# Kernel optimization log

Hardware: AMD Instinct MI355X
Metric: run time of the kernel (lower is better)

Reference implementation:

```python
import jax, jax.numpy as jnp
import numpy as np
from jax import lax

C = 512
B, T, N = 8, 16, 32
KSZ = 7
NEG_SLOPE = 0.01
LN_EPS = 1e-5


def setup_inputs() -> dict:
    key = jax.random.key(0)
    ks = jax.random.split(key, 8)
    local_feat = jax.random.normal(ks[0], (B, T, N, C), dtype=jnp.float32)
    global_feat = jax.random.normal(ks[1], (B, C), dtype=jnp.float32)
    pos = jax.random.normal(ks[2], (B, T, N, 3), dtype=jnp.float32)
    # adj_weight: nn.Linear(C, C, bias=False), init eye_ (perturb slightly to keep interesting ties)
    W = jnp.eye(C, dtype=jnp.float32) + 0.01 * jax.random.normal(ks[3], (C, C), dtype=jnp.float32)
    # depthwise Conv1d(C, C, 7, groups=C): weight [C, 1, 7], kaiming init; bias zeros
    conv_w = jax.random.normal(ks[4], (C, 1, KSZ), dtype=jnp.float32) * np.sqrt(2.0 / KSZ)
    conv_b = jnp.zeros((C,), dtype=jnp.float32)
    ln_gamma = jnp.ones((C,), dtype=jnp.float32)
    ln_beta = jnp.zeros((C,), dtype=jnp.float32)
    return {"local_feat": local_feat, "global_feat": global_feat, "pos": pos,
            "W": W, "conv_w": conv_w, "conv_b": conv_b,
            "ln_gamma": ln_gamma, "ln_beta": ln_beta}


def reference(local_feat, global_feat, pos, W, conv_w, conv_b, ln_gamma, ln_beta):
    b, t, nd, c = local_feat.shape
    n = t * nd
    feat = local_feat.reshape(b, n, c)
    # F.normalize(p=2, dim=-1, eps=1e-12)
    norm = feat / jnp.maximum(jnp.linalg.norm(feat, axis=-1, keepdims=True), 1e-12)
    # torch.einsum('bnc,cc,bcm->bnm'): repeated 'cc' takes the diagonal of W
    A = jnp.einsum('bnc,cc,bcm->bnm', norm, W, jnp.swapaxes(norm, 1, 2))
    A = A.reshape(b, n, t, nd)
    top_A = jnp.argmax(A, axis=-1)  # [b, n, t]
    # direct indexed gather -- avoids the [b, n, t, nd, c] stacked blowup
    top_feat = local_feat[jnp.arange(b)[:, None, None],
                          jnp.arange(t)[None, None, :],
                          top_A]                                 # [b, n, t, c]
    x = jnp.swapaxes(top_feat.reshape(b * n, t, c), 1, 2)        # [b*n, c, t]
    # depthwise conv1d, kernel 7, valid padding
    y = lax.conv_general_dilated(x, conv_w, window_strides=(1,), padding='VALID',
                                 dimension_numbers=('NCH', 'OIH', 'NCH'),
                                 feature_group_count=c)
    y = y + conv_b[None, :, None]                                # [b*n, c, t-6]
    y = jnp.swapaxes(y, 1, 2)                                    # [b*n, t-6, c]
    mu = jnp.mean(y, axis=-1, keepdims=True)
    var = jnp.mean(jnp.square(y - mu), axis=-1, keepdims=True)
    ln = (y - mu) * lax.rsqrt(var + LN_EPS) * ln_gamma + ln_beta
    act = jnp.where(ln >= 0, ln, NEG_SLOPE * ln)
    out = jnp.mean(act, axis=1)                                  # mean over time -> [b*n, c]
    return out.reshape(b, t, nd, c)
```

## Files before the change

### kernel.cpp

```cpp
#include <hip/hip_runtime.h>
#include <hip/hip_bf16.h>

#define C_DIM 512
#define B_DIM 8
#define T_DIM 16
#define ND_DIM 32
#define NPTS 512
#define ROWS 4096
#define KSZ 7
#define TOUT 10
#define NEG_SLOPE 0.01f
#define LN_EPS 1e-5f

__global__ __launch_bounds__(256) void norm_kernel(const float* __restrict__ feat,
                                                   float* __restrict__ nrm) {
    int row = blockIdx.x;
    int tid = threadIdx.x;
    const float* f = feat + (size_t)row * C_DIM;
    float* o = nrm + (size_t)row * C_DIM;
    float v0 = f[tid];
    float v1 = f[tid + 256];
    float ss = v0 * v0 + v1 * v1;
    #pragma unroll
    for (int off = 32; off > 0; off >>= 1) ss += __shfl_down(ss, off, 64);
    __shared__ float wsum[4];
    int wid = tid >> 6, lane = tid & 63;
    if (lane == 0) wsum[wid] = ss;
    __syncthreads();
    float tot = wsum[0] + wsum[1] + wsum[2] + wsum[3];
    float inv = 1.0f / fmaxf(sqrtf(tot), 1e-12f);
    o[tid] = v0 * inv;
    o[tid + 256] = v1 * inv;
}

__global__ __launch_bounds__(256, 1) void gemm_part_kernel(const float* __restrict__ nrm,
                                                           const float* __restrict__ W,
                                                           float* __restrict__ part) {
    __shared__ __align__(16) float As[2][128][20];
    __shared__ __align__(16) float Bs[2][128][20];
    __shared__ float wd[256];
    const int tid = threadIdx.x;
    const int tx = tid & 15, ty = tid >> 4;
    const int b = blockIdx.z >> 1, kz = blockIdx.z & 1;
    const int row0 = blockIdx.y * 128, col0 = blockIdx.x * 128;
    const int kbase = kz * 256;
    const float* __restrict__ Nb = nrm + (size_t)b * NPTS * C_DIM;

    wd[tid] = W[(size_t)(kbase + tid) * (C_DIM + 1)];
    __syncthreads();

    const int sr = tid >> 1;
    const int kh = (tid & 1) * 8;

    {
        const float* ga = Nb + (size_t)(row0 + sr) * C_DIM + kbase + kh;
        const float* gb = Nb + (size_t)(col0 + sr) * C_DIM + kbase + kh;
        float4 a0 = *(const float4*)ga, a1 = *(const float4*)(ga + 4);
        float4 b0 = *(const float4*)gb, b1 = *(const float4*)(gb + 4);
        float4 w0 = *(const float4*)&wd[kh], w1 = *(const float4*)&wd[kh + 4];
        a0.x *= w0.x; a0.y *= w0.y; a0.z *= w0.z; a0.w *= w0.w;
        a1.x *= w1.x; a1.y *= w1.y; a1.z *= w1.z; a1.w *= w1.w;
        *(float4*)&As[0][sr][kh] = a0; *(float4*)&As[0][sr][kh + 4] = a1;
        *(float4*)&Bs[0][sr][kh] = b0; *(float4*)&Bs[0][sr][kh + 4] = b1;
    }

    float acc[8][8] = {};
    #pragma unroll 1
    for (int step = 0; step < 16; ++step) {
        __syncthreads();
        const int buf = step & 1;
        if (step + 1 < 16) {
            const int koff = (step + 1) * 16;
            const float* ga = Nb + (size_t)(row0 + sr) * C_DIM + kbase + koff + kh;
            const float* gb = Nb + (size_t)(col0 + sr) * C_DIM + kbase + koff + kh;
            float4 a0 = *(const float4*)ga, a1 = *(const float4*)(ga + 4);
            float4 b0 = *(const float4*)gb, b1 = *(const float4*)(gb + 4);
            float4 w0 = *(const float4*)&wd[koff + kh], w1 = *(const float4*)&wd[koff + kh + 4];
            a0.x *= w0.x; a0.y *= w0.y; a0.z *= w0.z; a0.w *= w0.w;
            a1.x *= w1.x; a1.y *= w1.y; a1.z *= w1.z; a1.w *= w1.w;
            *(float4*)&As[buf ^ 1][sr][kh] = a0; *(float4*)&As[buf ^ 1][sr][kh + 4] = a1;
            *(float4*)&Bs[buf ^ 1][sr][kh] = b0; *(float4*)&Bs[buf ^ 1][sr][kh + 4] = b1;
        }
        #pragma unroll
        for (int k4 = 0; k4 < 4; ++k4) {
            float4 av[8], bv[8];
            #pragma unroll
            for (int i = 0; i < 8; i++) av[i] = *(const float4*)&As[buf][ty + 16 * i][k4 * 4];
            #pragma unroll
            for (int j = 0; j < 8; j++) bv[j] = *(const float4*)&Bs[buf][tx + 16 * j][k4 * 4];
            #pragma unroll
            for (int i = 0; i < 8; i++)
                #pragma unroll
                for (int j = 0; j < 8; j++)
                    acc[i][j] += av[i].x * bv[j].x + av[i].y * bv[j].y
                               + av[i].z * bv[j].z + av[i].w * bv[j].w;
        }
    }

    float* Cb = part + ((size_t)(kz * B_DIM + b) * NPTS + row0) * NPTS + col0;
    #pragma unroll
    for (int i = 0; i < 8; i++)
        #pragma unroll
        for (int j = 0; j < 8; j++)
            Cb[(size_t)(ty + 16 * i) * NPTS + tx + 16 * j] = acc[i][j];
}

__global__ __launch_bounds__(256) void reduce_argmax_kernel(const float* __restrict__ part,
                                                            int* __restrict__ idxg) {
    const int bn = blockIdx.x * 4 + (threadIdx.x >> 6);
    const int lane = threadIdx.x & 63;
    const float* p0 = part + (size_t)bn * NPTS + lane * 8;
    const float* p1 = part + (size_t)(ROWS + bn) * NPTS + lane * 8;
    float4 x0 = *(const float4*)p0, x1 = *(const float4*)(p0 + 4);
    float4 y0 = *(const float4*)p1, y1 = *(const float4*)(p1 + 4);
    float v[8] = { x0.x + y0.x, x0.y + y0.y, x0.z + y0.z, x0.w + y0.w,
                   x1.x + y1.x, x1.y + y1.y, x1.z + y1.z, x1.w + y1.w };
    float best = v[0];
    int bc = lane * 8;
    #pragma unroll
    for (int c = 1; c < 8; c++) {
        if (v[c] > best) { best = v[c]; bc = lane * 8 + c; }
    }
    #pragma unroll
    for (int m = 1; m < 4; m <<= 1) {
        float ov = __shfl_xor(best, m, 64);
        int oc = __shfl_xor(bc, m, 64);
        if (ov > best || (ov == best && oc < bc)) { best = ov; bc = oc; }
    }
    if ((lane & 3) == 0) idxg[(size_t)bn * T_DIM + (lane >> 2)] = bc & 31;
}

__global__ __launch_bounds__(256) void gemm_argmax_kernel(const float* __restrict__ nrm,
                                                          const float* __restrict__ W,
                                                          int* __restrict__ idxg) {
    __shared__ __align__(16) float As[16][68];
    __shared__ __align__(16) float Bs[16][68];
    __shared__ float Cs[64][65];
    __shared__ float wd[C_DIM];
    const int tid = threadIdx.x;
    const int tx = tid & 15, ty = tid >> 4;
    const int b = blockIdx.z;
    const int row0 = blockIdx.y * 64, col0 = blockIdx.x * 64;
    const float* Nb = nrm + (size_t)b * NPTS * C_DIM;

    wd[tid]       = W[(size_t)tid * (C_DIM + 1)];
    wd[tid + 256] = W[(size_t)(tid + 256) * (C_DIM + 1)];
    __syncthreads();

    float acc[4][4] = {};
    for (int k0 = 0; k0 < C_DIM; k0 += 16) {
        #pragma unroll
        for (int e = 0; e < 4; e++) {
            int idx = tid + e * 256;
            int m = idx >> 4, kk = idx & 15;
            As[kk][m] = Nb[(size_t)(row0 + m) * C_DIM + k0 + kk] * wd[k0 + kk];
            Bs[kk][m] = Nb[(size_t)(col0 + m) * C_DIM + k0 + kk];
        }
        __syncthreads();
        #pragma unroll
        for (int kk = 0; kk < 16; kk++) {
            float4 a4 = *(const float4*)&As[kk][ty * 4];
            float4 b4 = *(const float4*)&Bs[kk][tx * 4];
            float av[4] = {a4.x, a4.y, a4.z, a4.w};
            float bv[4] = {b4.x, b4.y, b4.z, b4.w};
            #pragma unroll
            for (int i = 0; i < 4; i++)
                #pragma unroll
                for (int j = 0; j < 4; j++)
                    acc[i][j] += av[i] * bv[j];
        }
        __syncthreads();
    }
    #pragma unroll
    for (int i = 0; i < 4; i++)
        #pragma unroll
        for (int j = 0; j < 4; j++)
            Cs[ty * 4 + i][tx * 4 + j] = acc[i][j];
    __syncthreads();
    if (tid < 128) {
        int r = tid >> 1, g = tid & 1;
        const float* crow = &Cs[r][g * 32];
        float best = crow[0];
        int bi = 0;
        for (int j = 1; j < 32; j++) {
            float v = crow[j];
            if (v > best) { best = v; bi = j; }
        }
        int n_glob = b * NPTS + row0 + r;
        int tg = (col0 >> 5) + g;
        idxg[(size_t)n_glob * T_DIM + tg] = bi;
    }
}

__global__ __launch_bounds__(256, 2) void fuse_kernel(const int* __restrict__ idxg,
                                                      const float* __restrict__ lf,
                                                      const float* __restrict__ cw,
                                                      const float* __restrict__ cb,
                                                      const float* __restrict__ gamma,
                                                      const float* __restrict__ beta,
                                                      float* __restrict__ out) {
    const int wave = threadIdx.x >> 6;
    const int lane = threadIdx.x & 63;
    const int bn = blockIdx.x * 4 + wave;
    const int b = bn >> 9;
    const int c0 = lane * 8;

    float x[T_DIM][8];
    #pragma unroll
    for (int t = 0; t < T_DIM; t++) {
        int idx = idxg[(size_t)bn * T_DIM + t];
        const float* p = lf + (((size_t)(b * T_DIM + t)) * ND_DIM + idx) * C_DIM + c0;
        float4 lo = *(const float4*)p;
        float4 hi = *(const float4*)(p + 4);
        x[t][0] = lo.x; x[t][1] = lo.y; x[t][2] = lo.z; x[t][3] = lo.w;
        x[t][4] = hi.x; x[t][5] = hi.y; x[t][6] = hi.z; x[t][7] = hi.w;
    }

    float w[KSZ][8];
    #pragma unroll
    for (int c = 0; c < 8; c++)
        #pragma unroll
        for (int k = 0; k < KSZ; k++)
            w[k][c] = cw[(size_t)(c0 + c) * KSZ + k];
    float bias[8], g[8], be[8];
    {
        float4 b_lo = *(const float4*)&cb[c0],    b_hi = *(const float4*)&cb[c0 + 4];
        float4 g_lo = *(const float4*)&gamma[c0], g_hi = *(const float4*)&gamma[c0 + 4];
        float4 e_lo = *(const float4*)&beta[c0],  e_hi = *(const float4*)&beta[c0 + 4];
        bias[0]=b_lo.x; bias[1]=b_lo.y; bias[2]=b_lo.z; bias[3]=b_lo.w;
        bias[4]=b_hi.x; bias[5]=b_hi.y; bias[6]=b_hi.z; bias[7]=b_hi.w;
        g[0]=g_lo.x; g[1]=g_lo.y; g[2]=g_lo.z; g[3]=g_lo.w;
        g[4]=g_hi.x; g[5]=g_hi.y; g[6]=g_hi.z; g[7]=g_hi.w;
        be[0]=e_lo.x; be[1]=e_lo.y; be[2]=e_lo.z; be[3]=e_lo.w;
        be[4]=e_hi.x; be[5]=e_hi.y; be[6]=e_hi.z; be[7]=e_hi.w;
    }

    float accum[8] = {};
    #pragma unroll
    for (int tau = 0; tau < TOUT; tau++) {
        float y[8];
        #pragma unroll
        for (int c = 0; c < 8; c++) {
            float v = bias[c];
            #pragma unroll
            for (int k = 0; k < KSZ; k++) v += x[tau + k][c] * w[k][c];
            y[c] = v;
        }
        float s = 0.f, q = 0.f;
        #pragma unroll
        for (int c = 0; c < 8; c++) { s += y[c]; q += y[c] * y[c]; }
        #pragma unroll
        for (int m = 1; m < 64; m <<= 1) {
            s += __shfl_xor(s, m, 64);
            q += __shfl_xor(q, m, 64);
        }
        float mu = s * (1.0f / 512.0f);
        float var = q * (1.0f / 512.0f) - mu * mu;
        float rs = rsqrtf(var + LN_EPS);
        #pragma unroll
        for (int c = 0; c < 8; c++) {
            float ln = (y[c] - mu) * rs * g[c] + be[c];
            accum[c] += ln >= 0.f ? ln : NEG_SLOPE * ln;
        }
    }
    float* o = out + (size_t)bn * C_DIM + c0;
    float4 r_lo = make_float4(accum[0]*0.1f, accum[1]*0.1f, accum[2]*0.1f, accum[3]*0.1f);
    float4 r_hi = make_float4(accum[4]*0.1f, accum[5]*0.1f, accum[6]*0.1f, accum[7]*0.1f);
    *(float4*)o = r_lo;
    *(float4*)(o + 4) = r_hi;
}

__global__ void sentinel_kernel(float* out, int n, float val) {
    int i = blockIdx.x * 256 + threadIdx.x;
    if (i < n) out[i] = val;
}

extern "C" void kernel_launch(void* const* d_in, const int* in_sizes, int n_in,
                              void* d_out, int out_size, void* d_ws, size_t ws_size,
                              hipStream_t stream) {
    const float* local_feat = (const float*)d_in[0];
    const float* W       = (const float*)d_in[3];
    const float* conv_w  = (const float*)d_in[4];
    const float* conv_b  = (const float*)d_in[5];
    const float* ln_g    = (const float*)d_in[6];
    const float* ln_b    = (const float*)d_in[7];
    float* out = (float*)d_out;

    (void)hipGetLastError();

    const size_t nrm_bytes  = (size_t)ROWS * C_DIM * sizeof(float);
    const size_t part_bytes = (size_t)2 * ROWS * NPTS * sizeof(float);
    const size_t idx_bytes  = (size_t)ROWS * T_DIM * sizeof(int);

    if (d_ws == nullptr || ws_size < nrm_bytes + idx_bytes) {
        float val = 512.0f + (float)(ws_size >> 20);
        sentinel_kernel<<<(out_size + 255) / 256, 256, 0, stream>>>(out, out_size, val);
        return;
    }

    float* nrm = (float*)d_ws;

    norm_kernel<<<ROWS, 256, 0, stream>>>(local_feat, nrm);

    int* idxg;
    if (ws_size >= nrm_bytes + part_bytes + idx_bytes) {
        float* part = (float*)((char*)d_ws + nrm_bytes);
        idxg = (int*)((char*)d_ws + nrm_bytes + part_bytes);
        gemm_part_kernel<<<dim3(NPTS / 128, NPTS / 128, B_DIM * 2), 256, 0, stream>>>(nrm, W, part);
        reduce_argmax_kernel<<<ROWS / 4, 256, 0, stream>>>(part, idxg);
    } else {
        idxg = (int*)((char*)d_ws + nrm_bytes);
        gemm_argmax_kernel<<<dim3(NPTS / 64, NPTS / 64, B_DIM), 256, 0, stream>>>(nrm, W, idxg);
    }

    fuse_kernel<<<ROWS / 4, 256, 0, stream>>>(idxg, local_feat, conv_w, conv_b,
                                              ln_g, ln_b, out);

    if (hipGetLastError() != hipSuccess) {
        hipMemsetAsync(d_out, 0x42, (size_t)out_size * 2, stream);
    }
}
```

Baseline: 150.7 us.

## Fold row normalization into GEMM loads and split K four ways

Replaces the normalized-feature materialization with a small kernel that computes only per-row inverse norms, which the GEMM applies while loading raw features. The K dimension is split four ways instead of two, doubling GEMM block count, and launch bounds now allow two blocks per CU. The reduce kernel sums four partial slices. This avoids writing and rereading the 8 MB normalized tensor but doubles the size of the partial-product buffer the reduce must read.

```diff
diff --git a/kernel.cpp b/kernel.cpp
--- a/kernel.cpp
+++ b/kernel.cpp
@@ -11,6 +11,21 @@
 #define TOUT 10
 #define NEG_SLOPE 0.01f
 #define LN_EPS 1e-5f
+#define KZ 4
+
+__global__ __launch_bounds__(256) void rnorm_kernel(const float* __restrict__ feat,
+                                                    float* __restrict__ rn) {
+    const int row = blockIdx.x * 4 + (threadIdx.x >> 6);
+    const int lane = threadIdx.x & 63;
+    const float* f = feat + (size_t)row * C_DIM + lane * 8;
+    float4 a = *(const float4*)f;
+    float4 b = *(const float4*)(f + 4);
+    float ss = a.x*a.x + a.y*a.y + a.z*a.z + a.w*a.w
+             + b.x*b.x + b.y*b.y + b.z*b.z + b.w*b.w;
+    #pragma unroll
+    for (int m = 1; m < 64; m <<= 1) ss += __shfl_xor(ss, m, 64);
+    if (lane == 0) rn[row] = 1.0f / fmaxf(sqrtf(ss), 1e-12f);
+}
 
 __global__ __launch_bounds__(256) void norm_kernel(const float* __restrict__ feat,
                                                    float* __restrict__ nrm) {
@@ -33,30 +48,36 @@
     o[tid + 256] = v1 * inv;
 }
 
-__global__ __launch_bounds__(256, 1) void gemm_part_kernel(const float* __restrict__ nrm,
+__global__ __launch_bounds__(256, 2) void gemm_part_kernel(const float* __restrict__ feat,
+                                                           const float* __restrict__ rn,
                                                            const float* __restrict__ W,
                                                            float* __restrict__ part) {
     __shared__ __align__(16) float As[2][128][20];
     __shared__ __align__(16) float Bs[2][128][20];
-    __shared__ float wd[256];
+    __shared__ float wd[128];
     const int tid = threadIdx.x;
     const int tx = tid & 15, ty = tid >> 4;
-    const int b = blockIdx.z >> 1, kz = blockIdx.z & 1;
+    const int b = blockIdx.z >> 2, kz = blockIdx.z & 3;
     const int row0 = blockIdx.y * 128, col0 = blockIdx.x * 128;
-    const int kbase = kz * 256;
-    const float* __restrict__ Nb = nrm + (size_t)b * NPTS * C_DIM;
-
-    wd[tid] = W[(size_t)(kbase + tid) * (C_DIM + 1)];
-    __syncthreads();
+    const int kbase = kz * 128;
+
+    if (tid < 128) wd[tid] = W[(size_t)(kbase + tid) * (C_DIM + 1)];
 
     const int sr = tid >> 1;
     const int kh = (tid & 1) * 8;
+    const float* __restrict__ fA = feat + (size_t)(b * NPTS + row0 + sr) * C_DIM + kbase + kh;
+    const float* __restrict__ fB = feat + (size_t)(b * NPTS + col0 + sr) * C_DIM + kbase + kh;
+    const float rna = rn[b * NPTS + row0 + sr];
+    const float rnb = rn[b * NPTS + col0 + sr];
+    __syncthreads();
 
     {
-        const float* ga = Nb + (size_t)(row0 + sr) * C_DIM + kbase + kh;
-        const float* gb = Nb + (size_t)(col0 + sr) * C_DIM + kbase + kh;
-        float4 a0 = *(const float4*)ga, a1 = *(const float4*)(ga + 4);
-        float4 b0 = *(const float4*)gb, b1 = *(const float4*)(gb + 4);
+        float4 a0 = *(const float4*)fA, a1 = *(const float4*)(fA + 4);
+        float4 b0 = *(const float4*)fB, b1 = *(const float4*)(fB + 4);
+        a0.x *= rna; a0.y *= rna; a0.z *= rna; a0.w *= rna;
+        a1.x *= rna; a1.y *= rna; a1.z *= rna; a1.w *= rna;
+        b0.x *= rnb; b0.y *= rnb; b0.z *= rnb; b0.w *= rnb;
+        b1.x *= rnb; b1.y *= rnb; b1.z *= rnb; b1.w *= rnb;
         float4 w0 = *(const float4*)&wd[kh], w1 = *(const float4*)&wd[kh + 4];
         a0.x *= w0.x; a0.y *= w0.y; a0.z *= w0.z; a0.w *= w0.w;
         a1.x *= w1.x; a1.y *= w1.y; a1.z *= w1.z; a1.w *= w1.w;
@@ -66,15 +87,17 @@
 
     float acc[8][8] = {};
     #pragma unroll 1
-    for (int step = 0; step < 16; ++step) {
+    for (int step = 0; step < 8; ++step) {
         __syncthreads();
         const int buf = step & 1;
-        if (step + 1 < 16) {
+        if (step + 1 < 8) {
             const int koff = (step + 1) * 16;
-            const float* ga = Nb + (size_t)(row0 + sr) * C_DIM + kbase + koff + kh;
-            const float* gb = Nb + (size_t)(col0 + sr) * C_DIM + kbase + koff + kh;
-            float4 a0 = *(const float4*)ga, a1 = *(const float4*)(ga + 4);
-            float4 b0 = *(const float4*)gb, b1 = *(const float4*)(gb + 4);
+            float4 a0 = *(const float4*)(fA + koff), a1 = *(const float4*)(fA + koff + 4);
+            float4 b0 = *(const float4*)(fB + koff), b1 = *(const float4*)(fB + koff + 4);
+            a0.x *= rna; a0.y *= rna; a0.z *= rna; a0.w *= rna;
+            a1.x *= rna; a1.y *= rna; a1.z *= rna; a1.w *= rna;
+            b0.x *= rnb; b0.y *= rnb; b0.z *= rnb; b0.w *= rnb;
+            b1.x *= rnb; b1.y *= rnb; b1.z *= rnb; b1.w *= rnb;
             float4 w0 = *(const float4*)&wd[koff + kh], w1 = *(const float4*)&wd[koff + kh + 4];
             a0.x *= w0.x; a0.y *= w0.y; a0.z *= w0.z; a0.w *= w0.w;
             a1.x *= w1.x; a1.y *= w1.y; a1.z *= w1.z; a1.w *= w1.w;
@@ -109,12 +132,16 @@
                                                             int* __restrict__ idxg) {
     const int bn = blockIdx.x * 4 + (threadIdx.x >> 6);
     const int lane = threadIdx.x & 63;
-    const float* p0 = part + (size_t)bn * NPTS + lane * 8;
-    const float* p1 = part + (size_t)(ROWS + bn) * NPTS + lane * 8;
-    float4 x0 = *(const float4*)p0, x1 = *(const float4*)(p0 + 4);
-    float4 y0 = *(const float4*)p1, y1 = *(const float4*)(p1 + 4);
-    float v[8] = { x0.x + y0.x, x0.y + y0.y, x0.z + y0.z, x0.w + y0.w,
-                   x1.x + y1.x, x1.y + y1.y, x1.z + y1.z, x1.w + y1.w };
+    const size_t base = (size_t)bn * NPTS + lane * 8;
+    const size_t slice = (size_t)ROWS * NPTS;
+    float4 s0a = *(const float4*)(part + base),             s0b = *(const float4*)(part + base + 4);
+    float4 s1a = *(const float4*)(part + slice + base),     s1b = *(const float4*)(part + slice + base + 4);
+    float4 s2a = *(const float4*)(part + 2 * slice + base), s2b = *(const float4*)(part + 2 * slice + base + 4);
+    float4 s3a = *(const float4*)(part + 3 * slice + base), s3b = *(const float4*)(part + 3 * slice + base + 4);
+    float v[8] = { ((s0a.x + s1a.x) + s2a.x) + s3a.x, ((s0a.y + s1a.y) + s2a.y) + s3a.y,
+                   ((s0a.z + s1a.z) + s2a.z) + s3a.z, ((s0a.w + s1a.w) + s2a.w) + s3a.w,
+                   ((s0b.x + s1b.x) + s2b.x) + s3b.x, ((s0b.y + s1b.y) + s2b.y) + s3b.y,
+                   ((s0b.z + s1b.z) + s2b.z) + s3b.z, ((s0b.w + s1b.w) + s2b.w) + s3b.w };
     float best = v[0];
     int bc = lane * 8;
     #pragma unroll
@@ -288,9 +315,11 @@
 
     (void)hipGetLastError();
 
+    const size_t rn_bytes   = 32768;
+    const size_t part4_bytes = (size_t)KZ * ROWS * NPTS * sizeof(float);
+    const size_t idx_bytes  = (size_t)ROWS * T_DIM * sizeof(int);
     const size_t nrm_bytes  = (size_t)ROWS * C_DIM * sizeof(float);
-    const size_t part_bytes = (size_t)2 * ROWS * NPTS * sizeof(float);
-    const size_t idx_bytes  = (size_t)ROWS * T_DIM * sizeof(int);
+    const size_t fast_need  = rn_bytes + part4_bytes + idx_bytes;
 
     if (d_ws == nullptr || ws_size < nrm_bytes + idx_bytes) {
         float val = 512.0f + (float)(ws_size >> 20);
@@ -298,18 +327,19 @@
         return;
     }
 
-    float* nrm = (float*)d_ws;
-
-    norm_kernel<<<ROWS, 256, 0, stream>>>(local_feat, nrm);
-
     int* idxg;
-    if (ws_size >= nrm_bytes + part_bytes + idx_bytes) {
-        float* part = (float*)((char*)d_ws + nrm_bytes);
-        idxg = (int*)((char*)d_ws + nrm_bytes + part_bytes);
-        gemm_part_kernel<<<dim3(NPTS / 128, NPTS / 128, B_DIM * 2), 256, 0, stream>>>(nrm, W, part);
+    if (ws_size >= fast_need) {
+        float* rnp  = (float*)d_ws;
+        float* part = (float*)((char*)d_ws + rn_bytes);
+        idxg = (int*)((char*)d_ws + rn_bytes + part4_bytes);
+        rnorm_kernel<<<ROWS / 4, 256, 0, stream>>>(local_feat, rnp);
+        gemm_part_kernel<<<dim3(NPTS / 128, NPTS / 128, B_DIM * KZ), 256, 0, stream>>>(
+            local_feat, rnp, W, part);
         reduce_argmax_kernel<<<ROWS / 4, 256, 0, stream>>>(part, idxg);
     } else {
+        float* nrm = (float*)d_ws;
         idxg = (int*)((char*)d_ws + nrm_bytes);
+        norm_kernel<<<ROWS, 256, 0, stream>>>(local_feat, nrm);
         gemm_argmax_kernel<<<dim3(NPTS / 64, NPTS / 64, B_DIM), 256, 0, stream>>>(nrm, W, idxg);
     }
 
```

Result: slower. 224.8 us (+49.2%).
